# Optimization experiments

Hardware: AMD Instinct MI355X
Metric: run time of the kernel (lower is better)

The kernel has to match this reference:

```python
import jax, jax.numpy as jnp
import numpy as np
import math

B, D, H, N, L = 32, 64, 8, 4096, 12
DK = D // H  # 8
APT = 10

def conv1x1_relu(x, w, b):
    # x: [B, C, N, L]; w: [O, C]; b: [O]  (1x1 conv == channel matmul)
    return jax.nn.relu(jnp.einsum('oc,bcnl->bonl', w, x) + b[None, :, None, None])

def setup_inputs() -> dict:
    key = jax.random.key(0)
    ks = jax.random.split(key, 12)
    s = 1.0 / math.sqrt(D)
    return {
        'x': jax.random.normal(ks[0], (B, D, N, L), jnp.float32),
        'wq': jax.random.normal(ks[1], (D, D), jnp.float32) * s,
        'bq': jnp.zeros((D,), jnp.float32),
        'wv': jax.random.normal(ks[2], (D, D), jnp.float32) * s,
        'bv': jnp.zeros((D,), jnp.float32),
        'wc': jax.random.normal(ks[3], (D, D), jnp.float32) * s,
        'bc': jnp.zeros((D,), jnp.float32),
        'memory': jax.random.normal(ks[4], (H, L, N, DK), jnp.float32) * 0.02,
        'weight': jnp.ones((D, N, L), jnp.float32),
        'bias': jnp.zeros((D, N, L), jnp.float32),
        'nv1': jax.random.normal(ks[5], (N, APT), jnp.float32),
        'nv2': jax.random.normal(ks[6], (APT, N), jnp.float32),
    }

def reference(x, wq, bq, wv, bv, wc, bc, memory, weight, bias, nv1, nv2):
    scale = 1.0 / math.sqrt(DK)
    q = conv1x1_relu(x, wq, bq)               # [B, D, N, L]
    v = conv1x1_relu(x, wv, bv)               # [B, D, N, L]
    # [B, D, N, L] -> [B, H, dk, N, L] -> [B, H, L, N, dk]
    v5 = jnp.transpose(v.reshape(B, H, DK, N, L), (0, 1, 4, 3, 2))
    q5 = jnp.transpose(q.reshape(B, H, DK, N, L), (0, 1, 4, 3, 2))
    key_sm = jax.nn.softmax(memory * scale, axis=-1)       # [H, L, N, dk]
    q_sm = jax.nn.softmax(q5 * scale, axis=-1)             # [B, H, L, N, dk]
    Aapt = jax.nn.softmax(jax.nn.relu(nv1 @ nv2), axis=-1) # [N, N]
    kv = jnp.einsum('hlnx,bhlny->bhlxy', key_sm, v5)       # [B,H,L,dk,dk]
    attn_qkv = jnp.einsum('bhlnx,bhlxy->bhlny', q_sm, kv)  # [B,H,L,N,dk]
    # 'nm,bhlnc->bhlnc' sums Aapt over m -> row-sum scaling of value
    row = jnp.sum(Aapt, axis=1)                            # [N]
    attn_dyn = row[None, None, None, :, None] * v5
    y = attn_qkv + attn_dyn                                # [B,H,L,N,dk]
    y = jnp.transpose(y, (0, 1, 4, 3, 2)).reshape(B, D, N, L)
    y = conv1x1_relu(y, wc, bc)
    out = y * weight[None] + bias[None] + y
    return out
```

## Files before the change

### kernel.cpp

```cpp
#include <hip/hip_runtime.h>
#include <math.h>

#define BB 32
#define DD 64
#define HH 8
#define NNN 4096
#define LL 12
#define PP (NNN * LL)
#define TILE 64
#define NTILES 24
#define CHUNK (TILE * NTILES)
#define NCHUNK (PP / CHUNK)
#define VSTRIDE 68
#define SCALE 0.35355339059327373f

__global__ void prep(const float* __restrict__ wq, const float* __restrict__ wv,
                     const float* __restrict__ wc, float* __restrict__ wt)
{
    const int i = blockIdx.x * 256 + threadIdx.x;
    const int o = i >> 6, c = i & 63;
    wt[c * 64 + o]        = wq[i];
    wt[4096 + c * 64 + o] = wv[i];
    wt[8192 + c * 64 + o] = wc[i];
}

__global__ __launch_bounds__(256, 4)
void pass_a(const float* __restrict__ x, const float* __restrict__ wvt,
            const float* __restrict__ bv, const float* __restrict__ mem,
            float* __restrict__ kv)
{
    __shared__ float v_tile[64 * VSTRIDE];
    __shared__ float ks_tile[64 * VSTRIDE];

    const int t = threadIdx.x;
    const int b = blockIdx.y;
    const int chunk0 = blockIdx.x * CHUNK;

    const int p1 = t & 63;
    const int og = t >> 6;
    const int o0 = og << 4;
    const int o0u = __builtin_amdgcn_readfirstlane(o0);
    const float* __restrict__ wvu = wvt + o0u;

    float bvl[16];
#pragma unroll
    for (int j = 0; j < 16; j++) bvl[j] = bv[o0 + j];

    const int h2 = t >> 5;
    const int x2 = (t >> 2) & 7;
    const int lsub = t & 3;

    float acc[3][8];
#pragma unroll
    for (int li = 0; li < 3; li++)
#pragma unroll
        for (int y = 0; y < 8; y++) acc[li][y] = 0.f;

    const float* xb = x + (size_t)(b * 64) * PP;

    for (int tile = 0; tile < NTILES; tile++) {
        const int pbase = chunk0 + tile * TILE;

#pragma unroll
        for (int i0 = 0; i0 < 2; i0++) {
            int i = t + i0 * 256;
            int pos = i >> 3, h = i & 7;
            int pg = pbase + pos;
            int n = pg / 12;
            int l = pg - n * 12;
            const float4* mp = (const float4*)(mem + (((size_t)(h * 12 + l) * NNN + n) << 3));
            float4 a0 = mp[0], a1 = mp[1];
            float v0 = a0.x * SCALE, v1 = a0.y * SCALE, v2 = a0.z * SCALE, v3 = a0.w * SCALE;
            float v4 = a1.x * SCALE, v5 = a1.y * SCALE, v6 = a1.z * SCALE, v7 = a1.w * SCALE;
            float m = fmaxf(fmaxf(fmaxf(v0, v1), fmaxf(v2, v3)),
                            fmaxf(fmaxf(v4, v5), fmaxf(v6, v7)));
            float e0 = __expf(v0 - m), e1 = __expf(v1 - m), e2 = __expf(v2 - m), e3 = __expf(v3 - m);
            float e4 = __expf(v4 - m), e5 = __expf(v5 - m), e6 = __expf(v6 - m), e7 = __expf(v7 - m);
            float inv = 1.0f / (e0 + e1 + e2 + e3 + e4 + e5 + e6 + e7);
            float4* kp = (float4*)(ks_tile + pos * VSTRIDE + (h << 3));
            kp[0] = make_float4(e0 * inv, e1 * inv, e2 * inv, e3 * inv);
            kp[1] = make_float4(e4 * inv, e5 * inv, e6 * inv, e7 * inv);
        }

        float va[16];
#pragma unroll
        for (int j = 0; j < 16; j++) va[j] = 0.f;
        const float* xp = xb + pbase + p1;
        for (int c = 0; c < 64; c += 4) {
            float xs0 = xp[(size_t)c * PP];
            float xs1 = xp[(size_t)(c + 1) * PP];
            float xs2 = xp[(size_t)(c + 2) * PP];
            float xs3 = xp[(size_t)(c + 3) * PP];
            const float* w0 = wvu + c * 64;
#pragma unroll
            for (int j = 0; j < 16; j++) {
                va[j] += w0[j] * xs0;
                va[j] += w0[64 + j] * xs1;
                va[j] += w0[128 + j] * xs2;
                va[j] += w0[192 + j] * xs3;
            }
        }
        float4* vt4 = (float4*)(v_tile + p1 * VSTRIDE + o0);
#pragma unroll
        for (int q4 = 0; q4 < 4; q4++) {
            float4 w;
            w.x = fmaxf(va[q4 * 4 + 0] + bvl[q4 * 4 + 0], 0.f);
            w.y = fmaxf(va[q4 * 4 + 1] + bvl[q4 * 4 + 1], 0.f);
            w.z = fmaxf(va[q4 * 4 + 2] + bvl[q4 * 4 + 2], 0.f);
            w.w = fmaxf(va[q4 * 4 + 3] + bvl[q4 * 4 + 3], 0.f);
            vt4[q4] = w;
        }
        __syncthreads();

        const int r = pbase % 12;
#pragma unroll
        for (int li = 0; li < 3; li++) {
            const int l = lsub * 3 + li;
            int s = l - r;
            if (s < 0) s += 12;
            for (int p = s; p < 64; p += 12) {
                float ksv = ks_tile[p * VSTRIDE + (h2 << 3) + x2];
                const float4* vp = (const float4*)(v_tile + p * VSTRIDE + (h2 << 3));
                float4 u0 = vp[0], u1 = vp[1];
                acc[li][0] += ksv * u0.x; acc[li][1] += ksv * u0.y;
                acc[li][2] += ksv * u0.z; acc[li][3] += ksv * u0.w;
                acc[li][4] += ksv * u1.x; acc[li][5] += ksv * u1.y;
                acc[li][6] += ksv * u1.z; acc[li][7] += ksv * u1.w;
            }
        }
        __syncthreads();
    }

#pragma unroll
    for (int li = 0; li < 3; li++) {
        const int l = lsub * 3 + li;
        float* kvp = kv + (((size_t)((b * 12 + l) * 8 + h2)) << 6) + (x2 << 3);
#pragma unroll
        for (int y = 0; y < 8; y++) atomicAdd(kvp + y, acc[li][y]);
    }
}

__global__ __launch_bounds__(256, 4)
void pass_b(const float* __restrict__ x, const float* __restrict__ wqt,
            const float* __restrict__ wvt, const float* __restrict__ wct,
            const float* __restrict__ bq, const float* __restrict__ bv,
            const float* __restrict__ bc, const float* __restrict__ kv,
            const float* __restrict__ wgt, const float* __restrict__ bsa,
            float* __restrict__ out)
{
    __shared__ float y_tile[64 * VSTRIDE];

    const int t = threadIdx.x;
    const int b = blockIdx.y;
    const int chunk0 = blockIdx.x * CHUNK;

    const int p1 = t & 63;
    const int og = t >> 6;
    const int o0 = og << 4;
    const int o0u = __builtin_amdgcn_readfirstlane(o0);
    const float* __restrict__ wqu = wqt + o0u;
    const float* __restrict__ wvu = wvt + o0u;
    const float* __restrict__ wcu = wct + o0u;

    float bql[16], bvl[16], bcl[16];
#pragma unroll
    for (int j = 0; j < 16; j++) {
        bql[j] = bq[o0 + j];
        bvl[j] = bv[o0 + j];
        bcl[j] = bc[o0 + j];
    }

    const float* xb = x + (size_t)(b * 64) * PP;
    float* ob = out + (size_t)(b * 64) * PP;

    for (int tile = 0; tile < NTILES; tile++) {
        const int pbase = chunk0 + tile * TILE;
        const int pg = pbase + p1;
        const int l = pg % 12;

        float qa[16], va[16];
#pragma unroll
        for (int j = 0; j < 16; j++) { qa[j] = 0.f; va[j] = 0.f; }
        const float* xp = xb + pg;
        for (int c = 0; c < 64; c += 4) {
            float xs0 = xp[(size_t)c * PP];
            float xs1 = xp[(size_t)(c + 1) * PP];
            float xs2 = xp[(size_t)(c + 2) * PP];
            float xs3 = xp[(size_t)(c + 3) * PP];
            const float* q0 = wqu + c * 64;
            const float* v0 = wvu + c * 64;
#pragma unroll
            for (int j = 0; j < 16; j++) {
                qa[j] += q0[j] * xs0;       va[j] += v0[j] * xs0;
                qa[j] += q0[64 + j] * xs1;  va[j] += v0[64 + j] * xs1;
                qa[j] += q0[128 + j] * xs2; va[j] += v0[128 + j] * xs2;
                qa[j] += q0[192 + j] * xs3; va[j] += v0[192 + j] * xs3;
            }
        }
#pragma unroll
        for (int j = 0; j < 16; j++) {
            qa[j] = fmaxf(qa[j] + bql[j], 0.f) * SCALE;
            va[j] = fmaxf(va[j] + bvl[j], 0.f);
        }

#pragma unroll
        for (int hh = 0; hh < 2; hh++) {
            float* qh = qa + hh * 8;
            float m = fmaxf(fmaxf(fmaxf(qh[0], qh[1]), fmaxf(qh[2], qh[3])),
                            fmaxf(fmaxf(qh[4], qh[5]), fmaxf(qh[6], qh[7])));
            float s = 0.f;
#pragma unroll
            for (int xk = 0; xk < 8; xk++) { qh[xk] = __expf(qh[xk] - m); s += qh[xk]; }
            float inv = 1.0f / s;
#pragma unroll
            for (int xk = 0; xk < 8; xk++) qh[xk] *= inv;
        }

#pragma unroll
        for (int hh = 0; hh < 2; hh++) {
            const int h = og * 2 + hh;
            const float* kvp = kv + (((size_t)((b * 12 + l) * 8 + h)) << 6);
            float yv[8];
#pragma unroll
            for (int y = 0; y < 8; y++) yv[y] = va[hh * 8 + y];
#pragma unroll
            for (int xk = 0; xk < 8; xk++) {
                float qv = qa[hh * 8 + xk];
                const float4* kp = (const float4*)(kvp + (xk << 3));
                float4 k0 = kp[0], k1 = kp[1];
                yv[0] += qv * k0.x; yv[1] += qv * k0.y;
                yv[2] += qv * k0.z; yv[3] += qv * k0.w;
                yv[4] += qv * k1.x; yv[5] += qv * k1.y;
                yv[6] += qv * k1.z; yv[7] += qv * k1.w;
            }
#pragma unroll
            for (int y = 0; y < 8; y++)
                y_tile[(o0 + hh * 8 + y) * VSTRIDE + p1] = yv[y];
        }
        __syncthreads();

        float ca[16];
#pragma unroll
        for (int j = 0; j < 16; j++) ca[j] = 0.f;
        for (int c = 0; c < 64; c += 4) {
            float y0 = y_tile[c * VSTRIDE + p1];
            float y1 = y_tile[(c + 1) * VSTRIDE + p1];
            float y2 = y_tile[(c + 2) * VSTRIDE + p1];
            float y3 = y_tile[(c + 3) * VSTRIDE + p1];
            const float* w0 = wcu + c * 64;
#pragma unroll
            for (int j = 0; j < 16; j++) {
                ca[j] += w0[j] * y0;
                ca[j] += w0[64 + j] * y1;
                ca[j] += w0[128 + j] * y2;
                ca[j] += w0[192 + j] * y3;
            }
        }
#pragma unroll
        for (int j = 0; j < 16; j++) {
            float yc = fmaxf(ca[j] + bcl[j], 0.f);
            size_t oi = (size_t)(o0 + j) * PP + pg;
            ob[oi] = yc * (wgt[oi] + 1.0f) + bsa[oi];
        }
        __syncthreads();
    }
}

extern "C" void kernel_launch(void* const* d_in, const int* in_sizes, int n_in,
                              void* d_out, int out_size, void* d_ws, size_t ws_size,
                              hipStream_t stream) {
    const float* x   = (const float*)d_in[0];
    const float* wq  = (const float*)d_in[1];
    const float* bq  = (const float*)d_in[2];
    const float* wv  = (const float*)d_in[3];
    const float* bv  = (const float*)d_in[4];
    const float* wc  = (const float*)d_in[5];
    const float* bc  = (const float*)d_in[6];
    const float* mem = (const float*)d_in[7];
    const float* wgt = (const float*)d_in[8];
    const float* bsa = (const float*)d_in[9];
    float* outp = (float*)d_out;

    float* kvw = (float*)d_ws;
    float* wt  = (float*)d_ws + (size_t)BB * LL * HH * 64;
    hipMemsetAsync(kvw, 0, (size_t)BB * LL * HH * 64 * sizeof(float), stream);

    prep<<<16, 256, 0, stream>>>(wq, wv, wc, wt);

    dim3 grid(NCHUNK, BB);
    pass_a<<<grid, 256, 0, stream>>>(x, wt + 4096, bv, mem, kvw);
    pass_b<<<grid, 256, 0, stream>>>(x, wt, wt + 4096, wt + 8192,
                                     bq, bv, bc, kvw, wgt, bsa, outp);
}
```

Baseline: 1.944 ms.

## Widen pass_a to 512 threads and halve pass_b chunk size

pass_a now runs 512 threads per block, so each thread computes 8 output channels instead of 16. The kv accumulation is remapped so every thread covers one or two sequence positions instead of three, and softmax loading is done in a single pass. pass_b now handles 12 tiles per block instead of 24, doubling its grid, and both kernels request higher occupancy through launch bounds. The aim is more parallelism and latency hiding, at the cost of more register pressure, divergence from the uneven l1 work split, and more atomics and per-block overhead.

```diff
diff --git a/kernel.cpp b/kernel.cpp
--- a/kernel.cpp
+++ b/kernel.cpp
@@ -7,10 +7,15 @@
 #define NNN 4096
 #define LL 12
 #define PP (NNN * LL)
-#define TILE 64
-#define NTILES 24
-#define CHUNK (TILE * NTILES)
-#define NCHUNK (PP / CHUNK)
+
+#define NTILES_A 24
+#define CHUNK_A (64 * NTILES_A)
+#define NCHUNK_A (PP / CHUNK_A)
+
+#define NTILES_B 12
+#define CHUNK_B (64 * NTILES_B)
+#define NCHUNK_B (PP / CHUNK_B)
+
 #define VSTRIDE 68
 #define SCALE 0.35355339059327373f
 
@@ -24,7 +29,7 @@
     wt[8192 + c * 64 + o] = wc[i];
 }
 
-__global__ __launch_bounds__(256, 4)
+__global__ __launch_bounds__(512, 8)
 void pass_a(const float* __restrict__ x, const float* __restrict__ wvt,
             const float* __restrict__ bv, const float* __restrict__ mem,
             float* __restrict__ kv)
@@ -34,37 +39,37 @@
 
     const int t = threadIdx.x;
     const int b = blockIdx.y;
-    const int chunk0 = blockIdx.x * CHUNK;
+    const int chunk0 = blockIdx.x * CHUNK_A;
 
     const int p1 = t & 63;
     const int og = t >> 6;
-    const int o0 = og << 4;
+    const int o0 = og << 3;
     const int o0u = __builtin_amdgcn_readfirstlane(o0);
     const float* __restrict__ wvu = wvt + o0u;
 
-    float bvl[16];
-#pragma unroll
-    for (int j = 0; j < 16; j++) bvl[j] = bv[o0 + j];
-
-    const int h2 = t >> 5;
-    const int x2 = (t >> 2) & 7;
-    const int lsub = t & 3;
-
-    float acc[3][8];
-#pragma unroll
-    for (int li = 0; li < 3; li++)
-#pragma unroll
-        for (int y = 0; y < 8; y++) acc[li][y] = 0.f;
+    float bvl[8];
+#pragma unroll
+    for (int j = 0; j < 8; j++) bvl[j] = bv[o0 + j];
+
+    const int h2 = (t >> 3) & 7;
+    const int x2 = t & 7;
+    const int l0 = t >> 6;
+    const int l1 = 8 + (t >> 6);
+    const bool has2 = (t < 256);
+
+    float acc[2][8];
+#pragma unroll
+    for (int q = 0; q < 2; q++)
+#pragma unroll
+        for (int y = 0; y < 8; y++) acc[q][y] = 0.f;
 
     const float* xb = x + (size_t)(b * 64) * PP;
 
-    for (int tile = 0; tile < NTILES; tile++) {
-        const int pbase = chunk0 + tile * TILE;
-
-#pragma unroll
-        for (int i0 = 0; i0 < 2; i0++) {
-            int i = t + i0 * 256;
-            int pos = i >> 3, h = i & 7;
+    for (int tile = 0; tile < NTILES_A; tile++) {
+        const int pbase = chunk0 + tile * 64;
+
+        {
+            int pos = t >> 3, h = t & 7;
             int pg = pbase + pos;
             int n = pg / 12;
             int l = pg - n * 12;
@@ -82,9 +87,9 @@
             kp[1] = make_float4(e4 * inv, e5 * inv, e6 * inv, e7 * inv);
         }
 
-        float va[16];
-#pragma unroll
-        for (int j = 0; j < 16; j++) va[j] = 0.f;
+        float va[8];
+#pragma unroll
+        for (int j = 0; j < 8; j++) va[j] = 0.f;
         const float* xp = xb + pbase + p1;
         for (int c = 0; c < 64; c += 4) {
             float xs0 = xp[(size_t)c * PP];
@@ -93,7 +98,7 @@
             float xs3 = xp[(size_t)(c + 3) * PP];
             const float* w0 = wvu + c * 64;
 #pragma unroll
-            for (int j = 0; j < 16; j++) {
+            for (int j = 0; j < 8; j++) {
                 va[j] += w0[j] * xs0;
                 va[j] += w0[64 + j] * xs1;
                 va[j] += w0[128 + j] * xs2;
@@ -101,46 +106,64 @@
             }
         }
         float4* vt4 = (float4*)(v_tile + p1 * VSTRIDE + o0);
-#pragma unroll
-        for (int q4 = 0; q4 < 4; q4++) {
+        {
             float4 w;
-            w.x = fmaxf(va[q4 * 4 + 0] + bvl[q4 * 4 + 0], 0.f);
-            w.y = fmaxf(va[q4 * 4 + 1] + bvl[q4 * 4 + 1], 0.f);
-            w.z = fmaxf(va[q4 * 4 + 2] + bvl[q4 * 4 + 2], 0.f);
-            w.w = fmaxf(va[q4 * 4 + 3] + bvl[q4 * 4 + 3], 0.f);
-            vt4[q4] = w;
+            w.x = fmaxf(va[0] + bvl[0], 0.f);
+            w.y = fmaxf(va[1] + bvl[1], 0.f);
+            w.z = fmaxf(va[2] + bvl[2], 0.f);
+            w.w = fmaxf(va[3] + bvl[3], 0.f);
+            vt4[0] = w;
+            w.x = fmaxf(va[4] + bvl[4], 0.f);
+            w.y = fmaxf(va[5] + bvl[5], 0.f);
+            w.z = fmaxf(va[6] + bvl[6], 0.f);
+            w.w = fmaxf(va[7] + bvl[7], 0.f);
+            vt4[1] = w;
         }
         __syncthreads();
 
         const int r = pbase % 12;
-#pragma unroll
-        for (int li = 0; li < 3; li++) {
-            const int l = lsub * 3 + li;
-            int s = l - r;
+        {
+            int s = l0 - r;
             if (s < 0) s += 12;
             for (int p = s; p < 64; p += 12) {
                 float ksv = ks_tile[p * VSTRIDE + (h2 << 3) + x2];
                 const float4* vp = (const float4*)(v_tile + p * VSTRIDE + (h2 << 3));
                 float4 u0 = vp[0], u1 = vp[1];
-                acc[li][0] += ksv * u0.x; acc[li][1] += ksv * u0.y;
-                acc[li][2] += ksv * u0.z; acc[li][3] += ksv * u0.w;
-                acc[li][4] += ksv * u1.x; acc[li][5] += ksv * u1.y;
-                acc[li][6] += ksv * u1.z; acc[li][7] += ksv * u1.w;
+                acc[0][0] += ksv * u0.x; acc[0][1] += ksv * u0.y;
+                acc[0][2] += ksv * u0.z; acc[0][3] += ksv * u0.w;
+                acc[0][4] += ksv * u1.x; acc[0][5] += ksv * u1.y;
+                acc[0][6] += ksv * u1.z; acc[0][7] += ksv * u1.w;
+            }
+        }
+        if (has2) {
+            int s = l1 - r;
+            if (s < 0) s += 12;
+            for (int p = s; p < 64; p += 12) {
+                float ksv = ks_tile[p * VSTRIDE + (h2 << 3) + x2];
+                const float4* vp = (const float4*)(v_tile + p * VSTRIDE + (h2 << 3));
+                float4 u0 = vp[0], u1 = vp[1];
+                acc[1][0] += ksv * u0.x; acc[1][1] += ksv * u0.y;
+                acc[1][2] += ksv * u0.z; acc[1][3] += ksv * u0.w;
+                acc[1][4] += ksv * u1.x; acc[1][5] += ksv * u1.y;
+                acc[1][6] += ksv * u1.z; acc[1][7] += ksv * u1.w;
             }
         }
         __syncthreads();
     }
 
-#pragma unroll
-    for (int li = 0; li < 3; li++) {
-        const int l = lsub * 3 + li;
-        float* kvp = kv + (((size_t)((b * 12 + l) * 8 + h2)) << 6) + (x2 << 3);
-#pragma unroll
-        for (int y = 0; y < 8; y++) atomicAdd(kvp + y, acc[li][y]);
+    {
+        float* kvp = kv + (((size_t)((b * 12 + l0) * 8 + h2)) << 6) + (x2 << 3);
+#pragma unroll
+        for (int y = 0; y < 8; y++) atomicAdd(kvp + y, acc[0][y]);
+    }
+    if (has2) {
+        float* kvp = kv + (((size_t)((b * 12 + l1) * 8 + h2)) << 6) + (x2 << 3);
+#pragma unroll
+        for (int y = 0; y < 8; y++) atomicAdd(kvp + y, acc[1][y]);
     }
 }
 
-__global__ __launch_bounds__(256, 4)
+__global__ __launch_bounds__(256, 8)
 void pass_b(const float* __restrict__ x, const float* __restrict__ wqt,
             const float* __restrict__ wvt, const float* __restrict__ wct,
             const float* __restrict__ bq, const float* __restrict__ bv,
@@ -152,7 +175,7 @@
 
     const int t = threadIdx.x;
     const int b = blockIdx.y;
-    const int chunk0 = blockIdx.x * CHUNK;
+    const int chunk0 = blockIdx.x * CHUNK_B;
 
     const int p1 = t & 63;
     const int og = t >> 6;
@@ -173,8 +196,8 @@
     const float* xb = x + (size_t)(b * 64) * PP;
     float* ob = out + (size_t)(b * 64) * PP;
 
-    for (int tile = 0; tile < NTILES; tile++) {
-        const int pbase = chunk0 + tile * TILE;
+    for (int tile = 0; tile < NTILES_B; tile++) {
+        const int pbase = chunk0 + tile * 64;
         const int pg = pbase + p1;
         const int l = pg % 12;
 
@@ -287,8 +310,9 @@
 
     prep<<<16, 256, 0, stream>>>(wq, wv, wc, wt);
 
-    dim3 grid(NCHUNK, BB);
-    pass_a<<<grid, 256, 0, stream>>>(x, wt + 4096, bv, mem, kvw);
-    pass_b<<<grid, 256, 0, stream>>>(x, wt, wt + 4096, wt + 8192,
-                                     bq, bv, bc, kvw, wgt, bsa, outp);
+    dim3 grid_a(NCHUNK_A, BB);
+    pass_a<<<grid_a, 512, 0, stream>>>(x, wt + 4096, bv, mem, kvw);
+    dim3 grid_b(NCHUNK_B, BB);
+    pass_b<<<grid_b, 256, 0, stream>>>(x, wt, wt + 4096, wt + 8192,
+                                       bq, bv, bc, kvw, wgt, bsa, outp);
 }
```

Measured after the change: 3.234 ms. 66.4% more time.
